# Kernel optimization log

Hardware: AMD Instinct MI355X
Metric: run time of the kernel (lower is better)

Reference implementation:

```python
import jax, jax.numpy as jnp
import numpy as np

NEG_SLOPE = 0.2
N_NODES = 50000


def gatv2_layer(x, src, dst, Wl, Wr, att, b, concat):
    # GATv2Conv (PyG semantics): x_l = lin_l(x) feeds messages (source side),
    # x_r = lin_r(x) is the target side; attention logit per edge/head is
    # att . leaky_relu(x_l[src] + x_r[dst]); softmax over incoming edges of dst.
    H, C = att.shape
    n = x.shape[0]
    xl = (x @ Wl).reshape(n, H, C)   # [N,H,C]
    xr = (x @ Wr).reshape(n, H, C)
    h = xl[src] + xr[dst]            # [E,H,C] gather
    logits = jnp.einsum('ehc,hc->eh', jax.nn.leaky_relu(h, NEG_SLOPE), att)  # [E,H]
    # segment softmax over target nodes
    m = jax.ops.segment_max(logits, dst, num_segments=n)
    m = jnp.where(jnp.isfinite(m), m, 0.0)
    ex = jnp.exp(logits - m[dst])
    s = jax.ops.segment_sum(ex, dst, num_segments=n)
    alpha = ex / (s[dst] + 1e-16)    # [E,H]
    msg = xl[src] * alpha[:, :, None]               # [E,H,C]
    out = jax.ops.segment_sum(msg, dst, num_segments=n)  # [N,H,C] scatter-add
    out = out.reshape(n, H * C) if concat else out.mean(axis=1)
    return out + b


def setup_inputs() -> dict:
    key = jax.random.key(0)
    ks = jax.random.split(key, 10)
    in_c, out_c, heads = 128, 64, 2
    node_fts = jax.random.normal(ks[0], (N_NODES, in_c), dtype=jnp.float32)
    edge_index = jax.random.randint(ks[1], (2, 800000), 0, N_NODES, dtype=jnp.int64)
    sc = 0.1
    return {
        'node_fts': node_fts,
        'edge_index': edge_index,
        'Wl1': jax.random.normal(ks[2], (in_c, heads * out_c), dtype=jnp.float32) * sc,
        'Wr1': jax.random.normal(ks[3], (in_c, heads * out_c), dtype=jnp.float32) * sc,
        'att1': jax.random.normal(ks[4], (heads, out_c), dtype=jnp.float32) * sc,
        'b1': jnp.zeros((heads * out_c,), dtype=jnp.float32),
        'Wl2': jax.random.normal(ks[5], (heads * out_c, out_c), dtype=jnp.float32) * sc,
        'Wr2': jax.random.normal(ks[6], (heads * out_c, out_c), dtype=jnp.float32) * sc,
        'att2': jax.random.normal(ks[7], (1, out_c), dtype=jnp.float32) * sc,
        'b2': jnp.zeros((out_c,), dtype=jnp.float32),
    }


def reference(node_fts, edge_index, Wl1, Wr1, att1, b1, Wl2, Wr2, att2, b2):
    n = node_fts.shape[0]
    loop = jnp.arange(n, dtype=edge_index.dtype)  # add_self_loops=True default
    src = jnp.concatenate([edge_index[0], loop])
    dst = jnp.concatenate([edge_index[1], loop])
    x = gatv2_layer(node_fts, src, dst, Wl1, Wr1, att1, b1, concat=True)
    x = jax.nn.relu(x)
    x = gatv2_layer(x, src, dst, Wl2, Wr2, att2, b2, concat=False)
    x = jax.nn.relu(x)
    return x
```

## Files before the change

kernel.cpp:

```cpp
#include <hip/hip_runtime.h>
#include <math.h>

typedef unsigned short ush;
typedef short bf16x8 __attribute__((ext_vector_type(8)));
typedef float f32x4 __attribute__((ext_vector_type(4)));
typedef ush ushx8 __attribute__((ext_vector_type(8)));

__device__ __forceinline__ ush f2bf(float f) {
    unsigned u = __float_as_uint(f);
    u += 0x7FFFu + ((u >> 16) & 1u);
    return (ush)(u >> 16);
}
__device__ __forceinline__ float bf2f(ush u) {
    return __uint_as_float((unsigned)u << 16);
}

__global__ __launch_bounds__(256) void fusedA_k(
    const int* __restrict__ dsts, int* __restrict__ ghist,
    const float* __restrict__ Wl1, const float* __restrict__ Wr1,
    const float* __restrict__ Wl2, const float* __restrict__ Wr2,
    ush* __restrict__ wph, ush* __restrict__ wpl, int e0, int etot) {
    const int t = threadIdx.x;
    if (blockIdx.x < 256) {
        __shared__ int h[512];
        for (int i = t; i < 512; i += 256) h[i] = 0;
        __syncthreads();
        for (int i = blockIdx.x * 256 + t; i < etot; i += 256 * 256) {
            const int d = (i < e0) ? dsts[i] : (i - e0);
            atomicAdd(&h[d >> 7], 1);
        }
        __syncthreads();
        for (int i = t; i < 512; i += 256)
            if (h[i]) atomicAdd(&ghist[i], h[i]);
    } else {
        const int bid = (blockIdx.x - 256) * 4 + (t >> 6);
        const int l = t & 63;
        const float* W;
        int C, fid;
        if (bid < 32)      { W = Wl1; C = 128; fid = bid; }
        else if (bid < 64) { W = Wr1; C = 128; fid = bid - 32; }
        else if (bid < 80) { W = Wl2; C = 64;  fid = bid - 64; }
        else               { W = Wr2; C = 64;  fid = bid - 80; }
        const int nc16 = C / 16;
        const int ks = fid / nc16, c16 = fid % nc16;
#pragma unroll
        for (int j = 0; j < 8; ++j) {
            const int k = ks * 32 + (l >> 4) * 8 + j;
            const int c = c16 * 16 + (l & 15);
            const float v = W[(size_t)k * C + c];
            const ush h = f2bf(v);
            wph[(size_t)(bid * 64 + l) * 8 + j] = h;
            wpl[(size_t)(bid * 64 + l) * 8 + j] = f2bf(v - bf2f(h));
        }
    }
}

__global__ __launch_bounds__(256) void fusedB_k(
    const int* __restrict__ srcs, const int* __restrict__ dsts,
    const int* __restrict__ ghist, int* __restrict__ cur, int* __restrict__ pairs,
    const float* __restrict__ x,
    const ush* __restrict__ wh1, const ush* __restrict__ wl1,
    const ush* __restrict__ wh2, const ush* __restrict__ wl2,
    ush* __restrict__ ybf, float* __restrict__ yf,
    int e0, int etot, int nblka, int n) {
    const int t = threadIdx.x;
    if ((int)blockIdx.x < nblka) {
        __shared__ int sb[512];
        __shared__ int red[256];
        __shared__ int hist[512], gbase[512], lcur[512];
        const int a0 = ghist[2 * t], a1 = ghist[2 * t + 1];
        red[t] = a0 + a1;
        __syncthreads();
#pragma unroll
        for (int s = 1; s < 256; s <<= 1) {
            const int add = (t >= s) ? red[t - s] : 0;
            __syncthreads();
            red[t] += add;
            __syncthreads();
        }
        const int base = red[t] - a0 - a1;
        sb[2 * t] = base;
        sb[2 * t + 1] = base + a0;
        for (int i = t; i < 512; i += 256) { hist[i] = 0; lcur[i] = 0; }
        __syncthreads();
        const int start = blockIdx.x * 2048;
        const int end = min(start + 2048, etot);
        for (int i = start + t; i < end; i += 256) {
            const int d = (i < e0) ? dsts[i] : (i - e0);
            atomicAdd(&hist[d >> 7], 1);
        }
        __syncthreads();
        for (int i = t; i < 512; i += 256) {
            const int c = hist[i];
            gbase[i] = c ? (sb[i] + atomicAdd(&cur[i], c)) : 0;
        }
        __syncthreads();
        for (int i = start + t; i < end; i += 256) {
            int s, d;
            if (i < e0) { s = srcs[i]; d = dsts[i]; } else { s = d = i - e0; }
            const int b = d >> 7;
            const int p = atomicAdd(&lcur[b], 1);
            pairs[gbase[b] + p] = s | ((d & 127) << 24);
        }
    } else {
        const int l = t & 63;
        const int w = t >> 6;
        const int r0 = ((int)blockIdx.x - nblka) * 64 + w * 16;
        const int arow = min(r0 + (l & 15), n - 1);
        const int kb = (l >> 4) * 8;
        bf16x8 ah[4], al[4];
#pragma unroll
        for (int ks = 0; ks < 4; ++ks) {
            const float* ap = x + (size_t)arow * 128 + ks * 32 + kb;
            const float4 v0 = *reinterpret_cast<const float4*>(ap);
            const float4 v1 = *reinterpret_cast<const float4*>(ap + 4);
            const float fv[8] = {v0.x, v0.y, v0.z, v0.w, v1.x, v1.y, v1.z, v1.w};
#pragma unroll
            for (int j = 0; j < 8; ++j) {
                const ush h = f2bf(fv[j]);
                ah[ks][j] = (short)h;
                al[ks][j] = (short)f2bf(fv[j] - bf2f(h));
            }
        }
        const int drow = (l >> 4) * 4;
        const int dcol = l & 15;
#pragma unroll
        for (int slab = 0; slab < 4; ++slab) {
            const bool isW1 = slab < 2;
            const int sl = slab & 1;
            const ush* __restrict__ wh = isW1 ? wh1 : wh2;
            const ush* __restrict__ wl = isW1 ? wl1 : wl2;
#pragma unroll
            for (int c16 = 0; c16 < 4; ++c16) {
                f32x4 acc = {0.f, 0.f, 0.f, 0.f};
#pragma unroll
                for (int ks = 0; ks < 4; ++ks) {
                    const int fid = ks * 8 + sl * 4 + c16;
                    const bf16x8 bh = *reinterpret_cast<const bf16x8*>(wh + (size_t)(fid * 64 + l) * 8);
                    const bf16x8 bl = *reinterpret_cast<const bf16x8*>(wl + (size_t)(fid * 64 + l) * 8);
                    acc = __builtin_amdgcn_mfma_f32_16x16x32_bf16(ah[ks], bh, acc, 0, 0, 0);
                    acc = __builtin_amdgcn_mfma_f32_16x16x32_bf16(al[ks], bh, acc, 0, 0, 0);
                    acc = __builtin_amdgcn_mfma_f32_16x16x32_bf16(ah[ks], bl, acc, 0, 0, 0);
                }
                const int cg = sl * 64 + c16 * 16 + dcol;
#pragma unroll
                for (int q = 0; q < 4; ++q) {
                    const int gr = r0 + drow + q;
                    if (gr < n) {
                        if (isW1) ybf[(size_t)gr * 128 + cg] = f2bf(acc[q]);
                        else      yf[(size_t)gr * 128 + cg] = acc[q];
                    }
                }
            }
        }
    }
}

__global__ __launch_bounds__(256) void bucket_fill2_k(
    const int* __restrict__ pairs, const int* __restrict__ ghist,
    int* __restrict__ row_ptr, int* __restrict__ csr_src,
    int* __restrict__ order, int n, int etot) {
    __shared__ int sb[512];
    __shared__ int red[256];
    __shared__ int cnt[128], cur[128], hcnt[128], horg[128], hcur[128];
    const int b = blockIdx.x, t = threadIdx.x;
    const int a0 = ghist[2 * t], a1 = ghist[2 * t + 1];
    red[t] = a0 + a1;
    __syncthreads();
#pragma unroll
    for (int s = 1; s < 256; s <<= 1) {
        const int add = (t >= s) ? red[t - s] : 0;
        __syncthreads();
        red[t] += add;
        __syncthreads();
    }
    const int base = red[t] - a0 - a1;
    sb[2 * t] = base;
    sb[2 * t + 1] = base + a0;
    if (t < 128) { cnt[t] = 0; hcnt[t] = 0; hcur[t] = 0; }
    __syncthreads();
    const int lo = sb[b];
    const int hi = (b + 1 < 512) ? sb[b + 1] : etot;
    for (int e = lo + t; e < hi; e += 256)
        atomicAdd(&cnt[(pairs[e] >> 24) & 127], 1);
    __syncthreads();
    const int x = (t < 128) ? cnt[t] : 0;
#pragma unroll
    for (int s = 1; s < 128; s <<= 1) {
        const int add = (t < 128 && t >= s) ? cnt[t - s] : 0;
        __syncthreads();
        if (t < 128) cnt[t] += add;
        __syncthreads();
    }
    int key = 0;
    bool valid = false;
    if (t < 128) {
        const int excl = cnt[t] - x;
        cur[t] = excl;
        const int d = b * 128 + t;
        if (d < n) {
            valid = true;
            row_ptr[d] = lo + excl;
            key = 127 - min(x, 127);
            atomicAdd(&hcnt[key], 1);
        }
    }
    if (b == 0 && t == 0) row_ptr[n] = etot;
    __syncthreads();
    if (t < 128) horg[t] = hcnt[t];
    __syncthreads();
#pragma unroll
    for (int s = 1; s < 128; s <<= 1) {
        const int add = (t < 128 && t >= s) ? hcnt[t - s] : 0;
        __syncthreads();
        if (t < 128) hcnt[t] += add;
        __syncthreads();
    }
    if (valid) {
        const int pos = (hcnt[key] - horg[key]) + atomicAdd(&hcur[key], 1);
        order[b * 128 + pos] = b * 128 + t;
    }
    __syncthreads();
    for (int e = lo + t; e < hi; e += 256) {
        const int p = pairs[e];
        const int pos = atomicAdd(&cur[(p >> 24) & 127], 1);
        csr_src[lo + pos] = p & 0xFFFFFF;
    }
}

__global__ __launch_bounds__(256) void gemm2_k(
    const ush* __restrict__ ahi, const ush* __restrict__ alo,
    const ush* __restrict__ whl, const ush* __restrict__ wll,
    const ush* __restrict__ whr, const ush* __restrict__ wlr,
    ush* __restrict__ ybf, float* __restrict__ yf, int n) {
    const int l = threadIdx.x & 63;
    const int w = threadIdx.x >> 6;
    const int r0 = blockIdx.x * 64 + w * 16;
    const int arow = min(r0 + (l & 15), n - 1);
    const int kb = (l >> 4) * 8;
    bf16x8 ah[4], al[4];
#pragma unroll
    for (int ks = 0; ks < 4; ++ks) {
        ah[ks] = *reinterpret_cast<const bf16x8*>(ahi + (size_t)arow * 128 + ks * 32 + kb);
        al[ks] = *reinterpret_cast<const bf16x8*>(alo + (size_t)arow * 128 + ks * 32 + kb);
    }
    const int drow = (l >> 4) * 4;
    const int dcol = l & 15;
#pragma unroll
    for (int slab = 0; slab < 2; ++slab) {
        const ush* __restrict__ wh = slab ? whr : whl;
        const ush* __restrict__ wl = slab ? wlr : wll;
#pragma unroll
        for (int c16 = 0; c16 < 4; ++c16) {
            f32x4 acc = {0.f, 0.f, 0.f, 0.f};
#pragma unroll
            for (int ks = 0; ks < 4; ++ks) {
                const int fid = ks * 4 + c16;
                const bf16x8 bh = *reinterpret_cast<const bf16x8*>(wh + (size_t)(fid * 64 + l) * 8);
                const bf16x8 bl = *reinterpret_cast<const bf16x8*>(wl + (size_t)(fid * 64 + l) * 8);
                acc = __builtin_amdgcn_mfma_f32_16x16x32_bf16(ah[ks], bh, acc, 0, 0, 0);
                acc = __builtin_amdgcn_mfma_f32_16x16x32_bf16(al[ks], bh, acc, 0, 0, 0);
                acc = __builtin_amdgcn_mfma_f32_16x16x32_bf16(ah[ks], bl, acc, 0, 0, 0);
            }
            const int cg = c16 * 16 + dcol;
#pragma unroll
            for (int q = 0; q < 4; ++q) {
                const int gr = r0 + drow + q;
                if (gr < n) {
                    if (slab == 0) ybf[(size_t)gr * 64 + cg] = f2bf(acc[q]);
                    else           yf[(size_t)gr * 64 + cg] = acc[q];
                }
            }
        }
    }
}

__global__ __launch_bounds__(256) void gat_dst2_k(
    const ush* __restrict__ xl, const float* __restrict__ xr,
    const int* __restrict__ row_ptr, const int* __restrict__ csr_src,
    const int* __restrict__ order, const float* __restrict__ att,
    const float* __restrict__ bias, ush* __restrict__ h1hi,
    ush* __restrict__ h1lo, int n) {
    const int lane = threadIdx.x & 63;
    const int g = lane >> 4, il = lane & 15;
    const int w = (blockIdx.x * blockDim.x + threadIdx.x) >> 6;
    if (w >= n) return;
    const int d = order[w];

    float xv[8], av[8];
    {
        const float4* xp = reinterpret_cast<const float4*>(xr + (size_t)d * 128 + il * 8);
        const float4* ap = reinterpret_cast<const float4*>(att + il * 8);
        const float4 x0 = xp[0], x1 = xp[1], a0 = ap[0], a1 = ap[1];
        xv[0]=x0.x; xv[1]=x0.y; xv[2]=x0.z; xv[3]=x0.w;
        xv[4]=x1.x; xv[5]=x1.y; xv[6]=x1.z; xv[7]=x1.w;
        av[0]=a0.x; av[1]=a0.y; av[2]=a0.z; av[3]=a0.w;
        av[4]=a1.x; av[5]=a1.y; av[6]=a1.z; av[7]=a1.w;
    }
    const int rp0 = row_ptr[d], rp1 = row_ptr[d + 1];

    float s = 0.f;
    float acc[8] = {0.f, 0.f, 0.f, 0.f, 0.f, 0.f, 0.f, 0.f};
    int i = rp0 + g;
    for (; i + 4 < rp1; i += 8) {
        const int s0 = csr_src[i];
        const int s1 = csr_src[i + 4];
        const ushx8 u0 = *reinterpret_cast<const ushx8*>(xl + (((size_t)(unsigned)s0) << 7) + il * 8);
        const ushx8 u1 = *reinterpret_cast<const ushx8*>(xl + (((size_t)(unsigned)s1) << 7) + il * 8);
        float f0[8], f1[8], p0 = 0.f, p1 = 0.f;
#pragma unroll
        for (int j = 0; j < 8; ++j) {
            f0[j] = bf2f((ush)u0[j]);
            const float v = f0[j] + xv[j];
            p0 = fmaf(av[j], fmaxf(v, 0.2f * v), p0);
        }
#pragma unroll
        for (int j = 0; j < 8; ++j) {
            f1[j] = bf2f((ush)u1[j]);
            const float v = f1[j] + xv[j];
            p1 = fmaf(av[j], fmaxf(v, 0.2f * v), p1);
        }
        p0 += __shfl_xor(p0, 4, 64); p0 += __shfl_xor(p0, 2, 64); p0 += __shfl_xor(p0, 1, 64);
        p1 += __shfl_xor(p1, 4, 64); p1 += __shfl_xor(p1, 2, 64); p1 += __shfl_xor(p1, 1, 64);
        const float w0 = __expf(p0), w1 = __expf(p1);
        s += w0 + w1;
#pragma unroll
        for (int j = 0; j < 8; ++j) acc[j] = fmaf(w0, f0[j], fmaf(w1, f1[j], acc[j]));
    }
    if (i < rp1) {
        const int s0 = csr_src[i];
        const ushx8 u0 = *reinterpret_cast<const ushx8*>(xl + (((size_t)(unsigned)s0) << 7) + il * 8);
        float f0[8], p0 = 0.f;
#pragma unroll
        for (int j = 0; j < 8; ++j) {
            f0[j] = bf2f((ush)u0[j]);
            const float v = f0[j] + xv[j];
            p0 = fmaf(av[j], fmaxf(v, 0.2f * v), p0);
        }
        p0 += __shfl_xor(p0, 4, 64); p0 += __shfl_xor(p0, 2, 64); p0 += __shfl_xor(p0, 1, 64);
        const float w0 = __expf(p0);
        s += w0;
#pragma unroll
        for (int j = 0; j < 8; ++j) acc[j] = fmaf(w0, f0[j], acc[j]);
    }
#pragma unroll
    for (int off = 16; off <= 32; off <<= 1) {
        s += __shfl_xor(s, off, 64);
#pragma unroll
        for (int j = 0; j < 8; ++j) acc[j] += __shfl_xor(acc[j], off, 64);
    }
    if (g == 0) {
        const float inv = 1.f / (s + 1e-16f);
        float bv[8];
        {
            const float4* bp = reinterpret_cast<const float4*>(bias + il * 8);
            const float4 b0 = bp[0], b1 = bp[1];
            bv[0]=b0.x; bv[1]=b0.y; bv[2]=b0.z; bv[3]=b0.w;
            bv[4]=b1.x; bv[5]=b1.y; bv[6]=b1.z; bv[7]=b1.w;
        }
        ushx8 hh, ll;
#pragma unroll
        for (int j = 0; j < 8; ++j) {
            const float o = fmaxf(fmaf(acc[j], inv, bv[j]), 0.f);
            const ush h = f2bf(o);
            hh[j] = h;
            ll[j] = f2bf(o - bf2f(h));
        }
        *reinterpret_cast<ushx8*>(h1hi + (size_t)d * 128 + il * 8) = hh;
        *reinterpret_cast<ushx8*>(h1lo + (size_t)d * 128 + il * 8) = ll;
    }
}

__global__ __launch_bounds__(256) void gat_dst1_k(
    const ush* __restrict__ xl, const float* __restrict__ xr,
    const int* __restrict__ row_ptr, const int* __restrict__ csr_src,
    const int* __restrict__ order, const float* __restrict__ att,
    const float* __restrict__ bias, float* __restrict__ out, int n) {
    const int lane = threadIdx.x & 63;
    const int g = lane >> 3, il = lane & 7;
    const int w = (blockIdx.x * blockDim.x + threadIdx.x) >> 6;
    if (w >= n) return;
    const int d = order[w];

    float xv[8], av[8];
    {
        const float4* xp = reinterpret_cast<const float4*>(xr + (size_t)d * 64 + il * 8);
        const float4* ap = reinterpret_cast<const float4*>(att + il * 8);
        const float4 x0 = xp[0], x1 = xp[1], a0 = ap[0], a1 = ap[1];
        xv[0]=x0.x; xv[1]=x0.y; xv[2]=x0.z; xv[3]=x0.w;
        xv[4]=x1.x; xv[5]=x1.y; xv[6]=x1.z; xv[7]=x1.w;
        av[0]=a0.x; av[1]=a0.y; av[2]=a0.z; av[3]=a0.w;
        av[4]=a1.x; av[5]=a1.y; av[6]=a1.z; av[7]=a1.w;
    }
    const int rp0 = row_ptr[d], rp1 = row_ptr[d + 1];

    float s = 0.f;
    float acc[8] = {0.f, 0.f, 0.f, 0.f, 0.f, 0.f, 0.f, 0.f};
    int i = rp0 + g;
    for (; i + 8 < rp1; i += 16) {
        const int s0 = csr_src[i];
        const int s1 = csr_src[i + 8];
        const ushx8 u0 = *reinterpret_cast<const ushx8*>(xl + (((size_t)(unsigned)s0) << 6) + il * 8);
        const ushx8 u1 = *reinterpret_cast<const ushx8*>(xl + (((size_t)(unsigned)s1) << 6) + il * 8);
        float f0[8], f1[8], p0 = 0.f, p1 = 0.f;
#pragma unroll
        for (int j = 0; j < 8; ++j) {
            f0[j] = bf2f((ush)u0[j]);
            const float v = f0[j] + xv[j];
            p0 = fmaf(av[j], fmaxf(v, 0.2f * v), p0);
        }
#pragma unroll
        for (int j = 0; j < 8; ++j) {
            f1[j] = bf2f((ush)u1[j]);
            const float v = f1[j] + xv[j];
            p1 = fmaf(av[j], fmaxf(v, 0.2f * v), p1);
        }
        p0 += __shfl_xor(p0, 4, 64); p0 += __shfl_xor(p0, 2, 64); p0 += __shfl_xor(p0, 1, 64);
        p1 += __shfl_xor(p1, 4, 64); p1 += __shfl_xor(p1, 2, 64); p1 += __shfl_xor(p1, 1, 64);
        const float w0 = __expf(p0), w1 = __expf(p1);
        s += w0 + w1;
#pragma unroll
        for (int j = 0; j < 8; ++j) acc[j] = fmaf(w0, f0[j], fmaf(w1, f1[j], acc[j]));
    }
    if (i < rp1) {
        const int s0 = csr_src[i];
        const ushx8 u0 = *reinterpret_cast<const ushx8*>(xl + (((size_t)(unsigned)s0) << 6) + il * 8);
        float f0[8], p0 = 0.f;
#pragma unroll
        for (int j = 0; j < 8; ++j) {
            f0[j] = bf2f((ush)u0[j]);
            const float v = f0[j] + xv[j];
            p0 = fmaf(av[j], fmaxf(v, 0.2f * v), p0);
        }
        p0 += __shfl_xor(p0, 4, 64); p0 += __shfl_xor(p0, 2, 64); p0 += __shfl_xor(p0, 1, 64);
        const float w0 = __expf(p0);
        s += w0;
#pragma unroll
        for (int j = 0; j < 8; ++j) acc[j] = fmaf(w0, f0[j], acc[j]);
    }
#pragma unroll
    for (int off = 8; off <= 32; off <<= 1) {
        s += __shfl_xor(s, off, 64);
#pragma unroll
        for (int j = 0; j < 8; ++j) acc[j] += __shfl_xor(acc[j], off, 64);
    }
    if (g == 0) {
        const float inv = 1.f / (s + 1e-16f);
        float bv[8];
        {
            const float4* bp = reinterpret_cast<const float4*>(bias + il * 8);
            const float4 b0 = bp[0], b1 = bp[1];
            bv[0]=b0.x; bv[1]=b0.y; bv[2]=b0.z; bv[3]=b0.w;
            bv[4]=b1.x; bv[5]=b1.y; bv[6]=b1.z; bv[7]=b1.w;
        }
        float4 o0, o1;
        o0.x = fmaxf(fmaf(acc[0], inv, bv[0]), 0.f);
        o0.y = fmaxf(fmaf(acc[1], inv, bv[1]), 0.f);
        o0.z = fmaxf(fmaf(acc[2], inv, bv[2]), 0.f);
        o0.w = fmaxf(fmaf(acc[3], inv, bv[3]), 0.f);
        o1.x = fmaxf(fmaf(acc[4], inv, bv[4]), 0.f);
        o1.y = fmaxf(fmaf(acc[5], inv, bv[5]), 0.f);
        o1.z = fmaxf(fmaf(acc[6], inv, bv[6]), 0.f);
        o1.w = fmaxf(fmaf(acc[7], inv, bv[7]), 0.f);
        float4* op = reinterpret_cast<float4*>(out + (size_t)d * 64 + il * 8);
        op[0] = o0;
        op[1] = o1;
    }
}

extern "C" void kernel_launch(void* const* d_in, const int* in_sizes, int n_in,
                              void* d_out, int out_size, void* d_ws, size_t ws_size,
                              hipStream_t stream) {
    const float* x    = (const float*)d_in[0];
    const int*   ei   = (const int*)d_in[1];
    const float* Wl1  = (const float*)d_in[2];
    const float* Wr1  = (const float*)d_in[3];
    const float* att1 = (const float*)d_in[4];
    const float* b1   = (const float*)d_in[5];
    const float* Wl2  = (const float*)d_in[6];
    const float* Wr2  = (const float*)d_in[7];
    const float* att2 = (const float*)d_in[8];
    const float* b2   = (const float*)d_in[9];

    const int n    = in_sizes[0] / 128;
    const int e0   = in_sizes[1] / 2;
    const int etot = e0 + n;
    const int* srcs = ei;
    const int* dsts = ei + e0;

    float* ws = (float*)d_ws;
    ush*   h1hi = (ush*)ws;
    ush*   h1lo = (ush*)(ws + (size_t)n * 64);
    ush*   xlbf = (ush*)(ws + (size_t)n * 128);
    float* xr   = ws + (size_t)n * 192;
    int* row_ptr = (int*)(ws + (size_t)n * 320);
    int* ghist   = row_ptr + (n + 2);
    int* cur     = ghist + 512;
    int* order   = cur + 512;
    int* csr_src = order + n;
    int* pairs   = csr_src + etot;
    ush* wph     = (ush*)(pairs + etot);
    ush* wpl     = wph + 96 * 512;

    const int NB    = (n + 127) / 128;
    const int nblka = (etot + 2047) / 2048;
    const int gx    = (n + 63) / 64;

    hipMemsetAsync(ghist, 0, 1024 * sizeof(int), stream);
    fusedA_k<<<256 + 24, 256, 0, stream>>>(dsts, ghist, Wl1, Wr1, Wl2, Wr2,
                                           wph, wpl, e0, etot);
    fusedB_k<<<nblka + gx, 256, 0, stream>>>(
        srcs, dsts, ghist, cur, pairs, x,
        wph, wpl, wph + 32 * 512, wpl + 32 * 512, xlbf, xr,
        e0, etot, nblka, n);
    bucket_fill2_k<<<NB, 256, 0, stream>>>(pairs, ghist, row_ptr, csr_src,
                                           order, n, etot);
    gat_dst2_k<<<(n + 3) / 4, 256, 0, stream>>>(xlbf, xr, row_ptr, csr_src, order,
                                                att1, b1, h1hi, h1lo, n);
    gemm2_k<<<gx, 256, 0, stream>>>(h1hi, h1lo, wph + 64 * 512, wpl + 64 * 512,
                                    wph + 80 * 512, wpl + 80 * 512, xlbf, xr, n);
    gat_dst1_k<<<(n + 3) / 4, 256, 0, stream>>>(xlbf, xr, row_ptr, csr_src, order,
                                                att2, b2, (float*)d_out, n);
}
```

Measured before the change: 187.9 us.

## Globally sort destination nodes by degree for load-balanced GAT processing

Before, the degree-descending node order was computed only within each 128-node bucket. It now comes from a global degree histogram: per-bucket counts are accumulated into global bins, a one-block kernel scans the bins, and a scatter kernel writes a full degree-sorted node order. This should give the GAT aggregation kernels better balance across waves and blocks. The cost is two extra small kernel launches and atomic traffic on global bins, and consecutive nodes in the order become scattered in memory.

After: 181.6 us. -3.4%, faster.

```diff
diff --git a/kernel.cpp b/kernel.cpp
--- a/kernel.cpp
+++ b/kernel.cpp
@@ -159,10 +159,10 @@
 __global__ __launch_bounds__(256) void bucket_fill2_k(
     const int* __restrict__ pairs, const int* __restrict__ ghist,
     int* __restrict__ row_ptr, int* __restrict__ csr_src,
-    int* __restrict__ order, int n, int etot) {
+    int* __restrict__ dbin, int n, int etot) {
     __shared__ int sb[512];
     __shared__ int red[256];
-    __shared__ int cnt[128], cur[128], hcnt[128], horg[128], hcur[128];
+    __shared__ int cnt[128], cur[128], hcnt[128];
     const int b = blockIdx.x, t = threadIdx.x;
     const int a0 = ghist[2 * t], a1 = ghist[2 * t + 1];
     red[t] = a0 + a1;
@@ -177,7 +177,7 @@
     const int base = red[t] - a0 - a1;
     sb[2 * t] = base;
     sb[2 * t + 1] = base + a0;
-    if (t < 128) { cnt[t] = 0; hcnt[t] = 0; hcur[t] = 0; }
+    if (t < 128) { cnt[t] = 0; hcnt[t] = 0; }
     __syncthreads();
     const int lo = sb[b];
     const int hi = (b + 1 < 512) ? sb[b + 1] : etot;
@@ -192,39 +192,62 @@
         if (t < 128) cnt[t] += add;
         __syncthreads();
     }
-    int key = 0;
-    bool valid = false;
     if (t < 128) {
         const int excl = cnt[t] - x;
         cur[t] = excl;
         const int d = b * 128 + t;
         if (d < n) {
-            valid = true;
             row_ptr[d] = lo + excl;
-            key = 127 - min(x, 127);
-            atomicAdd(&hcnt[key], 1);
+            atomicAdd(&hcnt[127 - min(x, 127)], 1);
         }
     }
     if (b == 0 && t == 0) row_ptr[n] = etot;
     __syncthreads();
-    if (t < 128) horg[t] = hcnt[t];
-    __syncthreads();
-#pragma unroll
-    for (int s = 1; s < 128; s <<= 1) {
-        const int add = (t < 128 && t >= s) ? hcnt[t - s] : 0;
-        __syncthreads();
-        if (t < 128) hcnt[t] += add;
-        __syncthreads();
-    }
-    if (valid) {
-        const int pos = (hcnt[key] - horg[key]) + atomicAdd(&hcur[key], 1);
-        order[b * 128 + pos] = b * 128 + t;
-    }
-    __syncthreads();
+    if (t < 128 && hcnt[t]) atomicAdd(&dbin[t], hcnt[t]);
     for (int e = lo + t; e < hi; e += 256) {
         const int p = pairs[e];
         const int pos = atomicAdd(&cur[(p >> 24) & 127], 1);
         csr_src[lo + pos] = p & 0xFFFFFF;
+    }
+}
+
+__global__ __launch_bounds__(128) void deg_scan_k(const int* __restrict__ dbin,
+                                                  int* __restrict__ dcur) {
+    __shared__ int red[128];
+    const int t = threadIdx.x;
+    const int x = dbin[t];
+    red[t] = x;
+    __syncthreads();
+#pragma unroll
+    for (int s = 1; s < 128; s <<= 1) {
+        const int add = (t >= s) ? red[t - s] : 0;
+        __syncthreads();
+        red[t] += add;
+        __syncthreads();
+    }
+    dcur[t] = red[t] - x;
+}
+
+__global__ __launch_bounds__(256) void deg_scatter_k(const int* __restrict__ row_ptr,
+                                                     int* __restrict__ dcur,
+                                                     int* __restrict__ order, int n) {
+    __shared__ int h[128], gbase[128], lcur[128];
+    const int t = threadIdx.x;
+    if (t < 128) { h[t] = 0; lcur[t] = 0; }
+    __syncthreads();
+    const int d = blockIdx.x * 256 + t;
+    int bin = -1;
+    if (d < n) {
+        const int deg = row_ptr[d + 1] - row_ptr[d];
+        bin = 127 - min(deg, 127);
+        atomicAdd(&h[bin], 1);
+    }
+    __syncthreads();
+    if (t < 128) gbase[t] = h[t] ? atomicAdd(&dcur[t], h[t]) : 0;
+    __syncthreads();
+    if (d < n) {
+        const int p = atomicAdd(&lcur[bin], 1);
+        order[gbase[bin] + p] = d;
     }
 }
 
@@ -496,17 +519,20 @@
     int* row_ptr = (int*)(ws + (size_t)n * 320);
     int* ghist   = row_ptr + (n + 2);
     int* cur     = ghist + 512;
-    int* order   = cur + 512;
+    int* dbin    = cur + 512;
+    int* dcur    = dbin + 128;
+    int* order   = dcur + 128;
     int* csr_src = order + n;
     int* pairs   = csr_src + etot;
     ush* wph     = (ush*)(pairs + etot);
     ush* wpl     = wph + 96 * 512;
 
     const int NB    = (n + 127) / 128;
+    const int NDB   = (n + 255) / 256;
     const int nblka = (etot + 2047) / 2048;
     const int gx    = (n + 63) / 64;
 
-    hipMemsetAsync(ghist, 0, 1024 * sizeof(int), stream);
+    hipMemsetAsync(ghist, 0, 1152 * sizeof(int), stream);
     fusedA_k<<<256 + 24, 256, 0, stream>>>(dsts, ghist, Wl1, Wr1, Wl2, Wr2,
                                            wph, wpl, e0, etot);
     fusedB_k<<<nblka + gx, 256, 0, stream>>>(
@@ -514,7 +540,9 @@
         wph, wpl, wph + 32 * 512, wpl + 32 * 512, xlbf, xr,
         e0, etot, nblka, n);
     bucket_fill2_k<<<NB, 256, 0, stream>>>(pairs, ghist, row_ptr, csr_src,
-                                           order, n, etot);
+                                           dbin, n, etot);
+    deg_scan_k<<<1, 128, 0, stream>>>(dbin, dcur);
+    deg_scatter_k<<<NDB, 256, 0, stream>>>(row_ptr, dcur, order, n);
     gat_dst2_k<<<(n + 3) / 4, 256, 0, stream>>>(xlbf, xr, row_ptr, csr_src, order,
                                                 att1, b1, h1hi, h1lo, n);
     gemm2_k<<<gx, 256, 0, stream>>>(h1hi, h1lo, wph + 64 * 512, wpl + 64 * 512,
```
